# Optimization experiments

Hardware: AMD Instinct MI355X
Metric: run time of the kernel (lower is better)

The kernel has to match this reference:

```python
import jax, jax.numpy as jnp
import numpy as np

N_NODES = 100000
N_EDGES = 1600000
F_IN, H1, H2, N_CLS = 512, 180, 120, 40
NEG_SLOPE = 0.01  # F.leaky_relu default


def setup_inputs() -> dict:
    key = jax.random.key(0)
    ks = jax.random.split(key, 8)
    x = jax.random.normal(ks[0], (N_NODES, F_IN), dtype=jnp.float32)
    edge_index = jax.random.randint(ks[1], (2, N_EDGES), 0, N_NODES, dtype=jnp.int64)
    W1 = jax.random.normal(ks[2], (F_IN, H1), dtype=jnp.float32) / np.sqrt(F_IN)
    b1 = jnp.zeros((H1,), dtype=jnp.float32)
    W2 = jax.random.normal(ks[3], (H1, H2), dtype=jnp.float32) / np.sqrt(H1)
    b2 = jnp.zeros((H2,), dtype=jnp.float32)
    W3 = jax.random.normal(ks[4], (H2, N_CLS), dtype=jnp.float32) / np.sqrt(H2)
    b3 = jnp.zeros((N_CLS,), dtype=jnp.float32)
    return {"x": x, "edge_index": edge_index, "W1": W1, "b1": b1,
            "W2": W2, "b2": b2, "W3": W3, "b3": b3}


def _add_self_loops(edge_index, n):
    loop = jnp.arange(n, dtype=edge_index.dtype)
    src = jnp.concatenate([edge_index[0], loop])
    dst = jnp.concatenate([edge_index[1], loop])
    return src, dst


def _gcn_conv(h, src, dst, norm, W, b, n):
    # PyG GCNConv: linear transform first, then normalized scatter-add at dst.
    h = h @ W  # [N, out]
    msg = norm[:, None] * h[src]  # gather at source, per-edge scale
    out = jax.ops.segment_sum(msg, dst, num_segments=n)  # scatter-add at dest
    return out + b


def reference(x, edge_index, W1, b1, W2, b2, W3, b3):
    n = x.shape[0]
    src, dst = _add_self_loops(edge_index, n)
    # symmetric normalization deg^-1/2 * deg^-1/2 on self-loop-augmented graph
    ones = jnp.ones(dst.shape[0], dtype=x.dtype)
    deg = jax.ops.segment_sum(ones, dst, num_segments=n)
    dinv = jnp.where(deg > 0, jax.lax.rsqrt(deg), 0.0)
    norm = dinv[src] * dinv[dst]  # [E+N]

    h = _gcn_conv(x, src, dst, norm, W1, b1, n)
    h = jnp.where(h >= 0, h, NEG_SLOPE * h)
    h = _gcn_conv(h, src, dst, norm, W2, b2, n)
    h = jnp.where(h >= 0, h, NEG_SLOPE * h)
    logits = h @ W3 + b3
    return jax.nn.log_softmax(logits, axis=1)
```

## Files before the change

### kernel.cpp

```cpp
#include <hip/hip_runtime.h>
#include <math.h>

typedef __attribute__((ext_vector_type(8))) short short8;
typedef __attribute__((ext_vector_type(4))) float f32x4;

static constexpr int F_IN = 512;
static constexpr int H1V = 180, H1P = 192;
static constexpr int H2V = 120, H2P = 128;
static constexpr int NC  = 40,  NCP = 64;

__device__ inline unsigned f2bf(float f) {
    unsigned u = __float_as_uint(f);
    return (u + 0x7fffu + ((u >> 16) & 1u)) >> 16;
}
__device__ inline unsigned cvtpk(float lo, float hi) {
    unsigned r;
    asm("v_cvt_pk_bf16_f32 %0, %1, %2" : "=v"(r) : "v"(lo), "v"(hi));
    return r;
}
#define BLO(u) __uint_as_float((u) << 16)
#define BHI(u) __uint_as_float((u) & 0xffff0000u)

__device__ inline void gload_lds16(const void* gsrc, void* ldst) {
    __builtin_amdgcn_global_load_lds(
        (const __attribute__((address_space(1))) void*)gsrc,
        (__attribute__((address_space(3))) void*)ldst, 16, 0, 0);
}

__global__ void k_init(const int* __restrict__ ei, int* __restrict__ flag,
                       const float* __restrict__ W1, const float* __restrict__ W2,
                       const float* __restrict__ W3, const float* __restrict__ b1,
                       const float* __restrict__ b2, const float* __restrict__ b3,
                       unsigned short* __restrict__ W1s, unsigned short* __restrict__ W2s,
                       unsigned short* __restrict__ W3s, float* __restrict__ b1p,
                       float* __restrict__ b2p, float* __restrict__ b3p) {
    if (blockIdx.x < 16) {
        int i = blockIdx.x * 256 + threadIdx.x;
        if (ei[2 * i + 1] != 0) flag[0] = 1;
        return;
    }
    const int n1 = F_IN * H1P;
    const int n2 = n1 + H1P * H2P;
    const int n3 = n2 + H2P * NCP;
    const int n4 = n3 + H1P;
    const int n5 = n4 + H2P;
    const int n6 = n5 + NCP;
    int i = (blockIdx.x - 16) * 256 + threadIdx.x;
    if (i < n1) {
        int k = i / H1P, c = i % H1P;
        float v = (c < H1V) ? W1[k * H1V + c] : 0.0f;
        W1s[(size_t)(k >> 3) * H1P * 8 + c * 8 + (k & 7)] = (unsigned short)f2bf(v);
    } else if (i < n2) {
        int j = i - n1;
        int k = j / H2P, c = j % H2P;
        float v = (k < H1V && c < H2V) ? W2[k * H2V + c] : 0.0f;
        W2s[(size_t)(k >> 3) * H2P * 8 + c * 8 + (k & 7)] = (unsigned short)f2bf(v);
    } else if (i < n3) {
        int j = i - n2;
        int k = j / NCP, c = j % NCP;
        float v = (k < H2V && c < NC) ? W3[k * NC + c] : 0.0f;
        W3s[(size_t)(k >> 3) * NCP * 8 + c * 8 + (k & 7)] = (unsigned short)f2bf(v);
    } else if (i < n4) {
        int c = i - n3;
        b1p[c] = (c < H1V) ? b1[c] : 0.0f;
    } else if (i < n5) {
        int c = i - n4;
        b2p[c] = (c < H2V) ? b2[c] : 0.0f;
    } else if (i < n6) {
        int c = i - n5;
        b3p[c] = (c < NC) ? b3[c] : -1e30f;
    }
}

__global__ __launch_bounds__(256) void k_megaA(const float* __restrict__ X,
                                               const short8* __restrict__ Bs,
                                               signed char* __restrict__ Hq,
                                               float* __restrict__ sc, int M, int gb,
                                               const int* __restrict__ ei, int E,
                                               const int* __restrict__ flag,
                                               int* __restrict__ deg,
                                               int* __restrict__ dst32,
                                               uint2* __restrict__ sr,
                                               int interleave) {
    __shared__ float ldsf[6144];
    int bid;
    bool isGemm;
    if (interleave) {
        int g = blockIdx.x / 3, r = blockIdx.x % 3;
        if (r == 0) { isGemm = true; bid = g; }
        else        { isGemm = false; bid = g * 2 + r - 1; }
    } else {
        isGemm = (int)blockIdx.x < gb;
        bid = isGemm ? blockIdx.x : blockIdx.x - gb;
    }

    if (!isGemm) {
        int e = bid * 256 + threadIdx.x;
        if (e >= E) return;
        bool i64 = (flag[0] == 0);
        int s, d;
        if (i64) { s = ei[2 * e]; d = ei[2 * E + 2 * e]; }
        else     { s = ei[e];     d = ei[E + e]; }
        int r = atomicAdd(&deg[d], 1);
        dst32[e] = d;
        sr[e] = make_uint2((unsigned)s, (unsigned)r);
        return;
    }

    char* lds = (char*)ldsf;
    int t = threadIdx.x;
    int w = t >> 6, l = t & 63;
    int lr = l & 15, kg = l >> 4;
    int row0 = bid * 32;
    int colb = w * 48;

    f32x4 acc[2][3];
#pragma unroll
    for (int m = 0; m < 2; ++m)
#pragma unroll
        for (int nn = 0; nn < 3; ++nn) acc[m][nn] = (f32x4){0.f, 0.f, 0.f, 0.f};

    auto stage = [&](int kb, int buf) {
#pragma unroll
        for (int j = 0; j < 2; ++j) {
            int o = j * 4096 + t * 16;
            int row = o >> 8;
            int col4 = ((o >> 4) & 15) ^ (row & 15);
            int rowg = row0 + row;
            if (rowg >= M) rowg = M - 1;
            gload_lds16(X + (size_t)rowg * F_IN + kb + col4 * 4,
                        lds + buf * 8192 + j * 4096 + w * 1024);
        }
    };

    short8 breg[2][2][3];
    auto loadB = [&](int ts, int pp) {
#pragma unroll
        for (int kk = 0; kk < 2; ++kk)
#pragma unroll
            for (int nn = 0; nn < 3; ++nn)
                breg[pp][kk][nn] =
                    Bs[(size_t)(ts * 8 + kk * 4 + kg) * H1P + colb + nn * 16 + lr];
    };

    auto compute = [&](int cur, int pp) {
#pragma unroll
        for (int kk = 0; kk < 2; ++kk) {
            short8 a[2];
#pragma unroll
            for (int m = 0; m < 2; ++m) {
                int row = m * 16 + lr;
                char* base = lds + cur * 8192 + row * 256;
                int c0 = kk * 8 + kg * 2;
                float4 v0 = *(const float4*)(base + (((c0 + 0) ^ (row & 15)) * 16));
                float4 v1 = *(const float4*)(base + (((c0 + 1) ^ (row & 15)) * 16));
                union { unsigned u[4]; short8 s; } cu;
                cu.u[0] = cvtpk(v0.x, v0.y);
                cu.u[1] = cvtpk(v0.z, v0.w);
                cu.u[2] = cvtpk(v1.x, v1.y);
                cu.u[3] = cvtpk(v1.z, v1.w);
                a[m] = cu.s;
            }
#pragma unroll
            for (int m = 0; m < 2; ++m)
#pragma unroll
                for (int nn = 0; nn < 3; ++nn)
                    acc[m][nn] = __builtin_amdgcn_mfma_f32_16x16x32_bf16(
                        a[m], breg[pp][kk][nn], acc[m][nn], 0, 0, 0);
        }
    };

    stage(0, 0);
    stage(64, 1);
    loadB(0, 0);
    asm volatile("s_waitcnt vmcnt(8)" ::: "memory");
    __builtin_amdgcn_s_barrier();
    __builtin_amdgcn_sched_barrier(0);

#pragma unroll
    for (int ts = 0; ts < 8; ++ts) {
        if (ts < 6) stage((ts + 2) * 64, (ts + 2) % 3);
        if (ts < 7) loadB(ts + 1, (ts + 1) & 1);
        compute(ts % 3, ts & 1);
        if (ts < 7) {
            if (ts < 6) {
                asm volatile("s_waitcnt vmcnt(8)" ::: "memory");
            } else {
                asm volatile("s_waitcnt vmcnt(6)" ::: "memory");
            }
            __builtin_amdgcn_s_barrier();
            __builtin_amdgcn_sched_barrier(0);
        }
    }

    __syncthreads();
    float* rmaxp = (float*)lds;
#pragma unroll
    for (int m = 0; m < 2; ++m) {
#pragma unroll
        for (int j = 0; j < 4; ++j) {
            int rl = m * 16 + kg * 4 + j;
            float lm = 0.f;
#pragma unroll
            for (int nn = 0; nn < 3; ++nn)
                lm = fmaxf(lm, fabsf(acc[m][nn][j]));
#pragma unroll
            for (int d = 1; d < 16; d <<= 1)
                lm = fmaxf(lm, __shfl_xor(lm, d));
            if (lr == 0) rmaxp[rl * 4 + w] = lm;
        }
    }
    __syncthreads();
#pragma unroll
    for (int m = 0; m < 2; ++m) {
#pragma unroll
        for (int j = 0; j < 4; ++j) {
            int rl = m * 16 + kg * 4 + j;
            int grow = row0 + rl;
            if (grow >= M) continue;
            float rm = fmaxf(fmaxf(rmaxp[rl * 4 + 0], rmaxp[rl * 4 + 1]),
                             fmaxf(rmaxp[rl * 4 + 2], rmaxp[rl * 4 + 3]));
            float inv = (rm > 0.f) ? 127.0f / rm : 0.f;
            if (w == 0 && lr == 0) sc[grow] = rm * (1.0f / 127.0f);
#pragma unroll
            for (int nn = 0; nn < 3; ++nn) {
                float v = acc[m][nn][j] * inv;
                v = fminf(fmaxf(rintf(v), -127.f), 127.f);
                Hq[(size_t)grow * H1P + colb + nn * 16 + lr] = (signed char)(int)v;
            }
        }
    }
}

__global__ void k_scan1(const int* __restrict__ deg, int* __restrict__ rp,
                        int* __restrict__ bsum, float* __restrict__ dinv,
                        const float* __restrict__ sc, float* __restrict__ scd,
                        int n) {
    __shared__ int s[256];
    int t = threadIdx.x;
    int base = blockIdx.x * 1024 + t * 4;
    int v0 = (base + 0 < n) ? deg[base + 0] : 0;
    int v1 = (base + 1 < n) ? deg[base + 1] : 0;
    int v2 = (base + 2 < n) ? deg[base + 2] : 0;
    int v3 = (base + 3 < n) ? deg[base + 3] : 0;
    if (base + 0 < n) { float d = rsqrtf((float)(v0 + 1)); dinv[base + 0] = d; scd[base + 0] = d * sc[base + 0]; }
    if (base + 1 < n) { float d = rsqrtf((float)(v1 + 1)); dinv[base + 1] = d; scd[base + 1] = d * sc[base + 1]; }
    if (base + 2 < n) { float d = rsqrtf((float)(v2 + 1)); dinv[base + 2] = d; scd[base + 2] = d * sc[base + 2]; }
    if (base + 3 < n) { float d = rsqrtf((float)(v3 + 1)); dinv[base + 3] = d; scd[base + 3] = d * sc[base + 3]; }
    int sum = v0 + v1 + v2 + v3;
    s[t] = sum;
    __syncthreads();
    for (int off = 1; off < 256; off <<= 1) {
        int x = (t >= off) ? s[t - off] : 0;
        __syncthreads();
        s[t] += x;
        __syncthreads();
    }
    int run = s[t] - sum;
    if (t == 255) bsum[blockIdx.x] = s[255];
    if (base + 0 < n) rp[base + 0] = run; run += v0;
    if (base + 1 < n) rp[base + 1] = run; run += v1;
    if (base + 2 < n) rp[base + 2] = run; run += v2;
    if (base + 3 < n) rp[base + 3] = run;
}

__global__ void k_scan2(int* __restrict__ bsum, int nb) {
    __shared__ int s[128];
    int t = threadIdx.x;
    int v = (t < nb) ? bsum[t] : 0;
    s[t] = v;
    __syncthreads();
    for (int off = 1; off < 128; off <<= 1) {
        int x = (t >= off) ? s[t - off] : 0;
        __syncthreads();
        s[t] += x;
        __syncthreads();
    }
    if (t < nb) bsum[t] = s[t] - v;
}

__global__ void k_scan3(const int* __restrict__ bsum, int* __restrict__ rp,
                        int n, int E) {
    int i = blockIdx.x * 256 + threadIdx.x;
    if (i < n) {
        rp[i] = rp[i] + bsum[i >> 10];
    } else if (i == n) {
        rp[n] = E;
    }
}

__global__ __launch_bounds__(256) void k_fill(const int* __restrict__ dst32,
                                              const uint2* __restrict__ sr, int E,
                                              const int* __restrict__ rp,
                                              int* __restrict__ csr,
                                              int bw, int chunk) {
    int bkt = blockIdx.x & 7;
    int lo = bkt * bw, hi = lo + bw;
    int ch = blockIdx.x >> 3;
    int e0 = ch * chunk;
    int e1 = min(E, e0 + chunk);
    for (int e = e0 + (int)threadIdx.x; e < e1; e += 256) {
        int d = dst32[e];
        if (d >= lo && d < hi) {
            uint2 v = sr[e];
            csr[rp[d] + (int)v.y] = (int)v.x;
        }
    }
}

__global__ __launch_bounds__(256) void k_gat1q(const signed char* __restrict__ Hq,
                                               const float* __restrict__ scd,
                                               const float* __restrict__ dinv,
                                               const int* __restrict__ rp,
                                               const int* __restrict__ csr,
                                               const float* __restrict__ bias,
                                               uint2* __restrict__ out, int n) {
    int wv = threadIdx.x >> 6, l = threadIdx.x & 63;
    int i = blockIdx.x * 4 + wv;
    if (i >= n) return;
    bool act = l < 48;
    int c = act ? l : 0;
    const unsigned* Hr = (const unsigned*)(Hq + c * 4);

    float a0, a1, a2, a3;
    {
        unsigned w0 = Hr[(size_t)i * 48];
        float s0 = scd[i];
        a0 = (float)(signed char)(w0) * s0;
        a1 = (float)(signed char)(w0 >> 8) * s0;
        a2 = (float)(signed char)(w0 >> 16) * s0;
        a3 = (float)(signed char)(w0 >> 24) * s0;
    }
    float p0 = 0.f, p1 = 0.f, p2 = 0.f, p3 = 0.f;

    int e0 = rp[i], e1 = rp[i + 1];
    int e = e0;
    for (; e + 7 < e1; e += 8) {
        int s[8];
#pragma unroll
        for (int q = 0; q < 8; ++q) s[q] = csr[e + q];
        float scs[8];
#pragma unroll
        for (int q = 0; q < 8; ++q) scs[q] = scd[s[q]];
        unsigned v[8];
#pragma unroll
        for (int q = 0; q < 8; ++q) v[q] = Hr[(size_t)s[q] * 48];
#pragma unroll
        for (int q = 0; q < 8; q += 2) {
            a0 = fmaf((float)(signed char)(v[q]), scs[q], a0);
            a1 = fmaf((float)(signed char)(v[q] >> 8), scs[q], a1);
            a2 = fmaf((float)(signed char)(v[q] >> 16), scs[q], a2);
            a3 = fmaf((float)(signed char)(v[q] >> 24), scs[q], a3);
            p0 = fmaf((float)(signed char)(v[q + 1]), scs[q + 1], p0);
            p1 = fmaf((float)(signed char)(v[q + 1] >> 8), scs[q + 1], p1);
            p2 = fmaf((float)(signed char)(v[q + 1] >> 16), scs[q + 1], p2);
            p3 = fmaf((float)(signed char)(v[q + 1] >> 24), scs[q + 1], p3);
        }
    }
    for (; e < e1; ++e) {
        int s0 = csr[e];
        float sq = scd[s0];
        unsigned w0 = Hr[(size_t)s0 * 48];
        a0 = fmaf((float)(signed char)(w0), sq, a0);
        a1 = fmaf((float)(signed char)(w0 >> 8), sq, a1);
        a2 = fmaf((float)(signed char)(w0 >> 16), sq, a2);
        a3 = fmaf((float)(signed char)(w0 >> 24), sq, a3);
    }
    a0 += p0; a1 += p1; a2 += p2; a3 += p3;

    float di = dinv[i];
    float4 bb = *(const float4*)(bias + 4 * c);
    float o0 = fmaf(di, a0, bb.x);
    float o1 = fmaf(di, a1, bb.y);
    float o2 = fmaf(di, a2, bb.z);
    float o3 = fmaf(di, a3, bb.w);
    o0 = o0 >= 0.f ? o0 : 0.01f * o0;
    o1 = o1 >= 0.f ? o1 : 0.01f * o1;
    o2 = o2 >= 0.f ? o2 : 0.01f * o2;
    o3 = o3 >= 0.f ? o3 : 0.01f * o3;
    if (act) {
        uint2 r;
        r.x = (f2bf(o1) << 16) | f2bf(o0);
        r.y = (f2bf(o3) << 16) | f2bf(o2);
        out[(size_t)i * 48 + c] = r;
    }
}

__global__ __launch_bounds__(512) void k_gemm2(const unsigned short* __restrict__ A,
                                               const short8* __restrict__ Bs,
                                               const float* __restrict__ dinv,
                                               unsigned short* __restrict__ Hout,
                                               int M) {
    __shared__ unsigned short ldsu[16384];
    char* lds = (char*)ldsu;
    int t = threadIdx.x;
    int w = t >> 6, l = t & 63;
    int lr = l & 15, kg = l >> 4;
    int wr = w >> 2, wc = w & 3;
    int row0 = blockIdx.x * 128;
    int colb = wc * 32;

    f32x4 acc[4][2];
#pragma unroll
    for (int m = 0; m < 4; ++m)
#pragma unroll
        for (int nn = 0; nn < 2; ++nn) acc[m][nn] = (f32x4){0.f, 0.f, 0.f, 0.f};

    auto stage = [&](int kb, int buf) {
#pragma unroll
        for (int j = 0; j < 2; ++j) {
            int o = j * 8192 + t * 16;
            int row = o >> 7;
            int chunk = ((o >> 4) & 7) ^ (row & 7);
            int rowg = row0 + row;
            if (rowg >= M) rowg = M - 1;
            gload_lds16(A + (size_t)rowg * H1P + kb + chunk * 8,
                        lds + buf * 16384 + j * 8192 + w * 1024);
        }
    };

    stage(0, 0);
    __syncthreads();

    for (int ts = 0; ts < 3; ++ts) {
        int cur = ts & 1;
        if (ts < 2) stage((ts + 1) * 64, cur ^ 1);
        short8 b[2][2];
#pragma unroll
        for (int kk = 0; kk < 2; ++kk)
#pragma unroll
            for (int nn = 0; nn < 2; ++nn)
                b[kk][nn] = Bs[(size_t)(ts * 8 + kk * 4 + kg) * H2P + colb + nn * 16 + lr];
        short8 a[2][4];
#pragma unroll
        for (int kk = 0; kk < 2; ++kk)
#pragma unroll
            for (int m = 0; m < 4; ++m) {
                int row = wr * 64 + m * 16 + lr;
                a[kk][m] = *(const short8*)(lds + cur * 16384 + row * 128 +
                                            (((kk * 4 + kg) ^ (row & 7)) * 16));
            }
#pragma unroll
        for (int kk = 0; kk < 2; ++kk)
#pragma unroll
            for (int m = 0; m < 4; ++m)
#pragma unroll
                for (int nn = 0; nn < 2; ++nn)
                    acc[m][nn] = __builtin_amdgcn_mfma_f32_16x16x32_bf16(a[kk][m], b[kk][nn], acc[m][nn], 0, 0, 0);
        __syncthreads();
    }

#pragma unroll
    for (int m = 0; m < 4; ++m) {
        int r4 = row0 + wr * 64 + m * 16 + kg * 4;
#pragma unroll
        for (int j = 0; j < 4; ++j) {
            int grow = r4 + j;
            if (grow < M) {
                float dv = dinv[grow];
#pragma unroll
                for (int nn = 0; nn < 2; ++nn)
                    Hout[(size_t)grow * H2P + colb + nn * 16 + lr] =
                        (unsigned short)f2bf(acc[m][nn][j] * dv);
            }
        }
    }
}

__global__ __launch_bounds__(256) void k_gat2(const uint2* __restrict__ H,
                                              const float* __restrict__ dinv,
                                              const int* __restrict__ rp,
                                              const int* __restrict__ csr,
                                              const float* __restrict__ bias,
                                              uint2* __restrict__ out, int n) {
    int wv = threadIdx.x >> 6, l = threadIdx.x & 63;
    int half = l >> 5, c = l & 31;
    int i = blockIdx.x * 8 + wv * 2 + half;
    if (i >= n) return;
    const uint2* Hr = H + c;

    float a0, a1, a2, a3;
    {
        uint2 v = Hr[(size_t)i * 32];
        a0 = BLO(v.x); a1 = BHI(v.x); a2 = BLO(v.y); a3 = BHI(v.y);
    }
    float p0 = 0.f, p1 = 0.f, p2 = 0.f, p3 = 0.f;

    int e0 = rp[i], e1 = rp[i + 1];
    int e = e0;
    for (; e + 7 < e1; e += 8) {
        int s[8];
#pragma unroll
        for (int q = 0; q < 8; ++q) s[q] = csr[e + q];
        uint2 v[8];
#pragma unroll
        for (int q = 0; q < 8; ++q) v[q] = Hr[(size_t)s[q] * 32];
#pragma unroll
        for (int q = 0; q < 8; q += 2) {
            a0 += BLO(v[q].x); a1 += BHI(v[q].x); a2 += BLO(v[q].y); a3 += BHI(v[q].y);
            p0 += BLO(v[q + 1].x); p1 += BHI(v[q + 1].x); p2 += BLO(v[q + 1].y); p3 += BHI(v[q + 1].y);
        }
    }
    for (; e + 3 < e1; e += 4) {
        int s0 = csr[e], s1 = csr[e + 1], s2 = csr[e + 2], s3 = csr[e + 3];
        uint2 va = Hr[(size_t)s0 * 32];
        uint2 vb = Hr[(size_t)s1 * 32];
        uint2 vc = Hr[(size_t)s2 * 32];
        uint2 vd = Hr[(size_t)s3 * 32];
        a0 += BLO(va.x); a1 += BHI(va.x); a2 += BLO(va.y); a3 += BHI(va.y);
        p0 += BLO(vb.x); p1 += BHI(vb.x); p2 += BLO(vb.y); p3 += BHI(vb.y);
        a0 += BLO(vc.x); a1 += BHI(vc.x); a2 += BLO(vc.y); a3 += BHI(vc.y);
        p0 += BLO(vd.x); p1 += BHI(vd.x); p2 += BLO(vd.y); p3 += BHI(vd.y);
    }
    for (; e < e1; ++e) {
        int s0 = csr[e];
        uint2 va = Hr[(size_t)s0 * 32];
        a0 += BLO(va.x); a1 += BHI(va.x); a2 += BLO(va.y); a3 += BHI(va.y);
    }
    a0 += p0; a1 += p1; a2 += p2; a3 += p3;

    float di = dinv[i];
    float4 bb = *(const float4*)(bias + 4 * c);
    float o0 = fmaf(di, a0, bb.x);
    float o1 = fmaf(di, a1, bb.y);
    float o2 = fmaf(di, a2, bb.z);
    float o3 = fmaf(di, a3, bb.w);
    o0 = o0 >= 0.f ? o0 : 0.01f * o0;
    o1 = o1 >= 0.f ? o1 : 0.01f * o1;
    o2 = o2 >= 0.f ? o2 : 0.01f * o2;
    o3 = o3 >= 0.f ? o3 : 0.01f * o3;
    uint2 r;
    r.x = (f2bf(o1) << 16) | f2bf(o0);
    r.y = (f2bf(o3) << 16) | f2bf(o2);
    out[(size_t)i * 32 + c] = r;
}

__global__ __launch_bounds__(256) void k_out(const unsigned short* __restrict__ H,
                                             const short8* __restrict__ Bs,
                                             const float* __restrict__ b3p,
                                             float* __restrict__ out, int M) {
    int t = threadIdx.x;
    int w = t >> 6, l = t & 63;
    int lr = l & 15, kg = l >> 4;
    int row0 = blockIdx.x * 64 + w * 16;

    f32x4 acc[4];
#pragma unroll
    for (int f = 0; f < 4; ++f) acc[f] = (f32x4){0.f, 0.f, 0.f, 0.f};

    int rowa = row0 + lr;
    if (rowa >= M) rowa = M - 1;
    const unsigned short* arow = H + (size_t)rowa * H2P;

#pragma unroll
    for (int ks = 0; ks < 4; ++ks) {
        short8 a = *(const short8*)(arow + ks * 32 + kg * 8);
#pragma unroll
        for (int f = 0; f < 4; ++f) {
            short8 b = Bs[(size_t)(ks * 4 + kg) * NCP + f * 16 + lr];
            acc[f] = __builtin_amdgcn_mfma_f32_16x16x32_bf16(a, b, acc[f], 0, 0, 0);
        }
    }

    float bl[4];
#pragma unroll
    for (int f = 0; f < 4; ++f) bl[f] = b3p[f * 16 + lr];

#pragma unroll
    for (int j = 0; j < 4; ++j) {
        int grow = row0 + kg * 4 + j;
        float lg[4];
#pragma unroll
        for (int f = 0; f < 4; ++f) lg[f] = acc[f][j] + bl[f];
        float m = fmaxf(fmaxf(lg[0], lg[1]), fmaxf(lg[2], lg[3]));
#pragma unroll
        for (int d = 1; d < 16; d <<= 1) m = fmaxf(m, __shfl_xor(m, d));
        float s = expf(lg[0] - m) + expf(lg[1] - m) + expf(lg[2] - m) + expf(lg[3] - m);
#pragma unroll
        for (int d = 1; d < 16; d <<= 1) s += __shfl_xor(s, d);
        float lse = m + logf(s);
        if (grow < M) {
#pragma unroll
            for (int f = 0; f < 4; ++f) {
                int c = f * 16 + lr;
                if (c < NC) out[(size_t)grow * NC + c] = lg[f] - lse;
            }
        }
    }
}

extern "C" void kernel_launch(void* const* d_in, const int* in_sizes, int n_in,
                              void* d_out, int out_size, void* d_ws, size_t ws_size,
                              hipStream_t stream) {
    const float* x  = (const float*)d_in[0];
    const int*   ei = (const int*)d_in[1];
    const float* W1 = (const float*)d_in[2];
    const float* b1 = (const float*)d_in[3];
    const float* W2 = (const float*)d_in[4];
    const float* b2 = (const float*)d_in[5];
    const float* W3 = (const float*)d_in[6];
    const float* b3 = (const float*)d_in[7];
    float* outp = (float*)d_out;

    int n = in_sizes[0] / F_IN;
    int E = in_sizes[1] / 2;

    char* p = (char*)d_ws;
    auto alloc = [&](size_t bytes) -> char* {
        char* r = p;
        p += (bytes + 511) & ~(size_t)511;
        return r;
    };
    int*            fd     = (int*)alloc((size_t)(n + 1) * 4);
    int*            flag   = fd;
    int*            deg    = fd + 1;
    float*          dinv   = (float*)alloc((size_t)n * 4);
    int*            rp     = (int*)alloc((size_t)(n + 1) * 4);
    int*            bsum   = (int*)alloc(4096);
    int*            dst32  = (int*)alloc((size_t)E * 4);
    uint2*          sr     = (uint2*)alloc((size_t)E * 8);
    int*            csr    = (int*)alloc((size_t)E * 4);
    unsigned short* W1s    = (unsigned short*)alloc((size_t)F_IN * H1P * 2);
    unsigned short* W2s    = (unsigned short*)alloc((size_t)H1P * H2P * 2);
    unsigned short* W3s    = (unsigned short*)alloc((size_t)H2P * NCP * 2);
    float*          b1p    = (float*)alloc(H1P * 4);
    float*          b2p    = (float*)alloc(H2P * 4);
    float*          b3p    = (float*)alloc(NCP * 4);
    signed char*    h1q    = (signed char*)alloc((size_t)n * H1P);
    float*          sc     = (float*)alloc((size_t)n * 4);
    float*          scd    = (float*)alloc((size_t)n * 4);
    unsigned short* h1agg  = (unsigned short*)alloc((size_t)n * H1P * 2);
    unsigned short* h2     = (unsigned short*)alloc((size_t)n * H2P * 2);
    unsigned short* h2agg  = (unsigned short*)alloc((size_t)n * H2P * 2);

    hipMemsetAsync(fd, 0, (size_t)(n + 1) * 4, stream);

    k_init<<<530, 256, 0, stream>>>(ei, flag, W1, W2, W3, b1, b2, b3,
                                    W1s, W2s, W3s, b1p, b2p, b3p);

    int gb = (n + 31) / 32;
    int eb = (E + 255) / 256;
    int interleave = (eb == 2 * gb) ? 1 : 0;
    k_megaA<<<gb + eb, 256, 0, stream>>>(x, (const short8*)W1s, h1q, sc, n, gb,
                                         ei, E, flag, deg, dst32, sr, interleave);

    int nb = (n + 1023) / 1024;
    k_scan1<<<nb, 256, 0, stream>>>(deg, rp, bsum, dinv, sc, scd, n);
    k_scan2<<<1, 128, 0, stream>>>(bsum, nb);
    k_scan3<<<(n + 1 + 255) / 256, 256, 0, stream>>>(bsum, rp, n, E);

    int bw = (n + 7) / 8;
    int nch = 256;
    int chunk = (E + nch - 1) / nch;
    k_fill<<<nch * 8, 256, 0, stream>>>(dst32, sr, E, rp, csr, bw, chunk);

    k_gat1q<<<(n + 3) / 4, 256, 0, stream>>>(h1q, scd, dinv, rp, csr, b1p,
                                             (uint2*)h1agg, n);
    k_gemm2<<<(n + 127) / 128, 512, 0, stream>>>(h1agg, (const short8*)W2s, dinv, h2, n);
    k_gat2<<<(n + 7) / 8, 256, 0, stream>>>((const uint2*)h2, dinv, rp, csr, b2p,
                                            (uint2*)h2agg, n);
    k_out<<<(n + 63) / 64, 256, 0, stream>>>(h2agg, (const short8*)W3s, b3p, outp, n);
}
```

Measured before the change: 317.5 us.

## Split node ranges to co-schedule gathers with GEMMs and fold scan2 into scan3

Splits the node range in half. The first-layer gather for the upper half now runs in the same launch as the layer-2 GEMM on the lower-half rows, and the second-layer gather for the upper half runs alongside the output GEMM and log-softmax on the lower half. The aim is to let the memory-bound CSR gathers overlap with the MFMA work instead of running as strictly serial kernels. The GEMM2 tile shrinks from 128 rows with 512 threads to 64 rows with 256 threads so both halves fit the same block shape. The block-sum scan is redundantly recomputed in every scan3 block, which saves one launch. The cost is more kernel launches overall and smaller GEMM tiles with less weight reuse.

```diff
diff --git a/kernel.cpp b/kernel.cpp
--- a/kernel.cpp
+++ b/kernel.cpp
@@ -264,26 +264,26 @@
     if (base + 3 < n) rp[base + 3] = run;
 }
 
-__global__ void k_scan2(int* __restrict__ bsum, int nb) {
-    __shared__ int s[128];
+__global__ void k_scan3(const int* __restrict__ bsum, int* __restrict__ rp,
+                        int n, int E, int nb) {
+    __shared__ int s[128], ov[128];
     int t = threadIdx.x;
-    int v = (t < nb) ? bsum[t] : 0;
-    s[t] = v;
+    if (t < 128) {
+        int v = (t < nb) ? bsum[t] : 0;
+        s[t] = v; ov[t] = v;
+    }
     __syncthreads();
     for (int off = 1; off < 128; off <<= 1) {
-        int x = (t >= off) ? s[t - off] : 0;
+        int x = 0;
+        if (t < 128 && t >= off) x = s[t - off];
         __syncthreads();
-        s[t] += x;
+        if (t < 128) s[t] += x;
         __syncthreads();
     }
-    if (t < nb) bsum[t] = s[t] - v;
-}
-
-__global__ void k_scan3(const int* __restrict__ bsum, int* __restrict__ rp,
-                        int n, int E) {
-    int i = blockIdx.x * 256 + threadIdx.x;
+    int i = blockIdx.x * 256 + t;
     if (i < n) {
-        rp[i] = rp[i] + bsum[i >> 10];
+        int b = i >> 10;
+        rp[i] += s[b] - ov[b];
     } else if (i == n) {
         rp[n] = E;
     }
@@ -308,15 +308,15 @@
     }
 }
 
-__global__ __launch_bounds__(256) void k_gat1q(const signed char* __restrict__ Hq,
-                                               const float* __restrict__ scd,
-                                               const float* __restrict__ dinv,
-                                               const int* __restrict__ rp,
-                                               const int* __restrict__ csr,
-                                               const float* __restrict__ bias,
-                                               uint2* __restrict__ out, int n) {
-    int wv = threadIdx.x >> 6, l = threadIdx.x & 63;
-    int i = blockIdx.x * 4 + wv;
+__device__ __forceinline__ void gat1q_body(int i, int tid,
+                                           const signed char* __restrict__ Hq,
+                                           const float* __restrict__ scd,
+                                           const float* __restrict__ dinv,
+                                           const int* __restrict__ rp,
+                                           const int* __restrict__ csr,
+                                           const float* __restrict__ bias,
+                                           uint2* __restrict__ out, int n) {
+    int l = tid & 63;
     if (i >= n) return;
     bool act = l < 48;
     int c = act ? l : 0;
@@ -386,19 +386,17 @@
     }
 }
 
-__global__ __launch_bounds__(512) void k_gemm2(const unsigned short* __restrict__ A,
-                                               const short8* __restrict__ Bs,
-                                               const float* __restrict__ dinv,
-                                               unsigned short* __restrict__ Hout,
-                                               int M) {
-    __shared__ unsigned short ldsu[16384];
-    char* lds = (char*)ldsu;
+__device__ __forceinline__ void gemm2_body(char* lds, int bid, int base,
+                                           const unsigned short* __restrict__ A,
+                                           const short8* __restrict__ Bs,
+                                           const float* __restrict__ dinv,
+                                           unsigned short* __restrict__ Hout,
+                                           int M) {
     int t = threadIdx.x;
     int w = t >> 6, l = t & 63;
     int lr = l & 15, kg = l >> 4;
-    int wr = w >> 2, wc = w & 3;
-    int row0 = blockIdx.x * 128;
-    int colb = wc * 32;
+    int row0 = base + bid * 64;
+    int colb = w * 32;
 
     f32x4 acc[4][2];
 #pragma unroll
@@ -409,13 +407,13 @@
     auto stage = [&](int kb, int buf) {
 #pragma unroll
         for (int j = 0; j < 2; ++j) {
-            int o = j * 8192 + t * 16;
+            int o = j * 4096 + t * 16;
             int row = o >> 7;
             int chunk = ((o >> 4) & 7) ^ (row & 7);
             int rowg = row0 + row;
             if (rowg >= M) rowg = M - 1;
             gload_lds16(A + (size_t)rowg * H1P + kb + chunk * 8,
-                        lds + buf * 16384 + j * 8192 + w * 1024);
+                        lds + buf * 8192 + o);
         }
     };
 
@@ -436,8 +434,8 @@
         for (int kk = 0; kk < 2; ++kk)
 #pragma unroll
             for (int m = 0; m < 4; ++m) {
-                int row = wr * 64 + m * 16 + lr;
-                a[kk][m] = *(const short8*)(lds + cur * 16384 + row * 128 +
+                int row = m * 16 + lr;
+                a[kk][m] = *(const short8*)(lds + cur * 8192 + row * 128 +
                                             (((kk * 4 + kg) ^ (row & 7)) * 16));
             }
 #pragma unroll
@@ -452,7 +450,7 @@
 
 #pragma unroll
     for (int m = 0; m < 4; ++m) {
-        int r4 = row0 + wr * 64 + m * 16 + kg * 4;
+        int r4 = row0 + m * 16 + kg * 4;
 #pragma unroll
         for (int j = 0; j < 4; ++j) {
             int grow = r4 + j;
@@ -467,15 +465,15 @@
     }
 }
 
-__global__ __launch_bounds__(256) void k_gat2(const uint2* __restrict__ H,
-                                              const float* __restrict__ dinv,
-                                              const int* __restrict__ rp,
-                                              const int* __restrict__ csr,
-                                              const float* __restrict__ bias,
-                                              uint2* __restrict__ out, int n) {
-    int wv = threadIdx.x >> 6, l = threadIdx.x & 63;
-    int half = l >> 5, c = l & 31;
-    int i = blockIdx.x * 8 + wv * 2 + half;
+__device__ __forceinline__ void gat2_body(int i, int tid,
+                                          const uint2* __restrict__ H,
+                                          const float* __restrict__ dinv,
+                                          const int* __restrict__ rp,
+                                          const int* __restrict__ csr,
+                                          const float* __restrict__ bias,
+                                          uint2* __restrict__ out, int n) {
+    int l = tid & 63;
+    int c = l & 31;
     if (i >= n) return;
     const uint2* Hr = H + c;
 
@@ -500,17 +498,6 @@
             a0 += BLO(v[q].x); a1 += BHI(v[q].x); a2 += BLO(v[q].y); a3 += BHI(v[q].y);
             p0 += BLO(v[q + 1].x); p1 += BHI(v[q + 1].x); p2 += BLO(v[q + 1].y); p3 += BHI(v[q + 1].y);
         }
-    }
-    for (; e + 3 < e1; e += 4) {
-        int s0 = csr[e], s1 = csr[e + 1], s2 = csr[e + 2], s3 = csr[e + 3];
-        uint2 va = Hr[(size_t)s0 * 32];
-        uint2 vb = Hr[(size_t)s1 * 32];
-        uint2 vc = Hr[(size_t)s2 * 32];
-        uint2 vd = Hr[(size_t)s3 * 32];
-        a0 += BLO(va.x); a1 += BHI(va.x); a2 += BLO(va.y); a3 += BHI(va.y);
-        p0 += BLO(vb.x); p1 += BHI(vb.x); p2 += BLO(vb.y); p3 += BHI(vb.y);
-        a0 += BLO(vc.x); a1 += BHI(vc.x); a2 += BLO(vc.y); a3 += BHI(vc.y);
-        p0 += BLO(vd.x); p1 += BHI(vd.x); p2 += BLO(vd.y); p3 += BHI(vd.y);
     }
     for (; e < e1; ++e) {
         int s0 = csr[e];
@@ -535,14 +522,15 @@
     out[(size_t)i * 32 + c] = r;
 }
 
-__global__ __launch_bounds__(256) void k_out(const unsigned short* __restrict__ H,
-                                             const short8* __restrict__ Bs,
-                                             const float* __restrict__ b3p,
-                                             float* __restrict__ out, int M) {
+__device__ __forceinline__ void kout_body(int bid, int base,
+                                          const unsigned short* __restrict__ H,
+                                          const short8* __restrict__ Bs,
+                                          const float* __restrict__ b3p,
+                                          float* __restrict__ out, int M) {
     int t = threadIdx.x;
     int w = t >> 6, l = t & 63;
     int lr = l & 15, kg = l >> 4;
-    int row0 = blockIdx.x * 64 + w * 16;
+    int row0 = base + bid * 64 + w * 16;
 
     f32x4 acc[4];
 #pragma unroll
@@ -586,6 +574,89 @@
                 if (c < NC) out[(size_t)grow * NC + c] = lg[f] - lse;
             }
         }
+    }
+}
+
+__global__ __launch_bounds__(256) void k_gat1q(const signed char* __restrict__ Hq,
+                                               const float* __restrict__ scd,
+                                               const float* __restrict__ dinv,
+                                               const int* __restrict__ rp,
+                                               const int* __restrict__ csr,
+                                               const float* __restrict__ bias,
+                                               uint2* __restrict__ out, int n,
+                                               int nbase) {
+    int i = nbase + blockIdx.x * 4 + (threadIdx.x >> 6);
+    gat1q_body(i, threadIdx.x, Hq, scd, dinv, rp, csr, bias, out, n);
+}
+
+__global__ __launch_bounds__(256) void k_gemm2(const unsigned short* __restrict__ A,
+                                               const short8* __restrict__ Bs,
+                                               const float* __restrict__ dinv,
+                                               unsigned short* __restrict__ Hout,
+                                               int M, int base) {
+    __shared__ char lds[16384];
+    gemm2_body(lds, blockIdx.x, base, A, Bs, dinv, Hout, M);
+}
+
+__global__ __launch_bounds__(256) void k_gat2(const uint2* __restrict__ H,
+                                              const float* __restrict__ dinv,
+                                              const int* __restrict__ rp,
+                                              const int* __restrict__ csr,
+                                              const float* __restrict__ bias,
+                                              uint2* __restrict__ out, int n,
+                                              int nbase) {
+    int l = threadIdx.x & 63;
+    int i = nbase + blockIdx.x * 8 + (threadIdx.x >> 6) * 2 + (l >> 5);
+    gat2_body(i, threadIdx.x, H, dinv, rp, csr, bias, out, n);
+}
+
+__global__ __launch_bounds__(256) void k_out(const unsigned short* __restrict__ H,
+                                             const short8* __restrict__ Bs,
+                                             const float* __restrict__ b3p,
+                                             float* __restrict__ out, int M, int base) {
+    kout_body(blockIdx.x, base, H, Bs, b3p, out, M);
+}
+
+__global__ __launch_bounds__(256) void k_megaB(const unsigned short* __restrict__ h1agg,
+                                               const short8* __restrict__ W2s,
+                                               const float* __restrict__ dinv,
+                                               unsigned short* __restrict__ h2,
+                                               int M, int g2b,
+                                               const signed char* __restrict__ Hq,
+                                               const float* __restrict__ scd,
+                                               const int* __restrict__ rp,
+                                               const int* __restrict__ csr,
+                                               const float* __restrict__ b1p,
+                                               uint2* __restrict__ h1aggout,
+                                               int nh) {
+    __shared__ char lds[16384];
+    if ((int)blockIdx.x < g2b) {
+        gemm2_body(lds, blockIdx.x, 0, h1agg, W2s, dinv, h2, M);
+    } else {
+        int bid = blockIdx.x - g2b;
+        int i = nh + bid * 4 + (threadIdx.x >> 6);
+        gat1q_body(i, threadIdx.x, Hq, scd, dinv, rp, csr, b1p, h1aggout, M);
+    }
+}
+
+__global__ __launch_bounds__(256) void k_megaC(const unsigned short* __restrict__ h2agg,
+                                               const short8* __restrict__ W3s,
+                                               const float* __restrict__ b3p,
+                                               float* __restrict__ out, int M, int kob,
+                                               const uint2* __restrict__ h2,
+                                               const float* __restrict__ dinv,
+                                               const int* __restrict__ rp,
+                                               const int* __restrict__ csr,
+                                               const float* __restrict__ b2p,
+                                               uint2* __restrict__ h2aggout,
+                                               int nh) {
+    if ((int)blockIdx.x < kob) {
+        kout_body(blockIdx.x, 0, h2agg, W3s, b3p, out, M);
+    } else {
+        int bid = blockIdx.x - kob;
+        int l = threadIdx.x & 63;
+        int i = nh + bid * 8 + (threadIdx.x >> 6) * 2 + (l >> 5);
+        gat2_body(i, threadIdx.x, h2, dinv, rp, csr, b2p, h2aggout, M);
     }
 }
 
@@ -646,18 +717,35 @@
 
     int nb = (n + 1023) / 1024;
     k_scan1<<<nb, 256, 0, stream>>>(deg, rp, bsum, dinv, sc, scd, n);
-    k_scan2<<<1, 128, 0, stream>>>(bsum, nb);
-    k_scan3<<<(n + 1 + 255) / 256, 256, 0, stream>>>(bsum, rp, n, E);
+    k_scan3<<<(n + 1 + 255) / 256, 256, 0, stream>>>(bsum, rp, n, E, nb);
 
     int bw = (n + 7) / 8;
     int nch = 256;
     int chunk = (E + nch - 1) / nch;
     k_fill<<<nch * 8, 256, 0, stream>>>(dst32, sr, E, rp, csr, bw, chunk);
 
-    k_gat1q<<<(n + 3) / 4, 256, 0, stream>>>(h1q, scd, dinv, rp, csr, b1p,
-                                             (uint2*)h1agg, n);
-    k_gemm2<<<(n + 127) / 128, 512, 0, stream>>>(h1agg, (const short8*)W2s, dinv, h2, n);
-    k_gat2<<<(n + 7) / 8, 256, 0, stream>>>((const uint2*)h2, dinv, rp, csr, b2p,
-                                            (uint2*)h2agg, n);
-    k_out<<<(n + 63) / 64, 256, 0, stream>>>(h2agg, (const short8*)W3s, b3p, outp, n);
-}
+    int nh = (n / 2) & ~7;
+    int g1lo = nh / 4;
+    int g1hi = (n - nh + 3) / 4;
+    int g2lo = nh / 64;
+    int g2hib = g2lo * 64;
+    int g2hi = (n - g2hib + 63) / 64;
+    int kolo = nh / 64;
+    int kohib = kolo * 64;
+    int kohi = (n - kohib + 63) / 64;
+    int gt2lo = nh / 8;
+    int gt2hi = (n - nh + 7) / 8;
+
+    k_gat1q<<<g1lo, 256, 0, stream>>>(h1q, scd, dinv, rp, csr, b1p,
+                                      (uint2*)h1agg, n, 0);
+    k_megaB<<<g2lo + g1hi, 256, 0, stream>>>(h1agg, (const short8*)W2s, dinv, h2,
+                                             n, g2lo, h1q, scd, rp, csr, b1p,
+                                             (uint2*)h1agg, nh);
+    k_gemm2<<<g2hi, 256, 0, stream>>>(h1agg, (const short8*)W2s, dinv, h2, n, g2hib);
+    k_gat2<<<gt2lo, 256, 0, stream>>>((const uint2*)h2, dinv, rp, csr, b2p,
+                                      (uint2*)h2agg, n, 0);
+    k_megaC<<<kolo + gt2hi, 256, 0, stream>>>(h2agg, (const short8*)W3s, b3p, outp,
+                                              n, kolo, (const uint2*)h2, dinv, rp,
+                                              csr, b2p, (uint2*)h2agg, nh);
+    k_out<<<kohi, 256, 0, stream>>>(h2agg, (const short8*)W3s, b3p, outp, n, kohib);
+}
```

Measured after the change: 361.9 us. +14.0%, slower.
